# Optimization experiments

Hardware: AMD Instinct MI355X
Metric: run time of the kernel (lower is better)

## Reference

```python
import jax, jax.numpy as jnp
import numpy as np

T, N, E, F0, F1 = 8, 100000, 3200000, 16, 16


def setup_inputs() -> dict:
    key = jax.random.key(0)
    ks = jax.random.split(key, 18)
    inp = {}
    inp["X"] = jax.random.normal(ks[0], (T, N, F0), jnp.float32)
    inp["edge_row"] = jax.random.randint(ks[1], (T, E), 0, N, jnp.int32)
    inp["edge_col"] = jax.random.randint(ks[2], (T, E), 0, N, jnp.int32)
    inp["edge_val"] = jax.random.uniform(ks[3], (T, E), jnp.float32)
    inp["p"] = jax.random.normal(ks[4], (F0,), jnp.float32)
    names = ["W_Z", "U_Z", "B_Z", "W_R", "U_R", "B_R", "W_H", "U_H", "B_H", "W_init"]
    for i, n in enumerate(names):
        inp[n] = jax.random.normal(ks[5 + i], (F0, F1 if n.startswith("B") or n == "W_init" else F0), jnp.float32)
    inp["lin_w"] = jax.random.normal(ks[15], (F1,), jnp.float32)
    inp["lin_b"] = jax.random.normal(ks[16], (1,), jnp.float32)
    return inp


def reference(X, edge_row, edge_col, edge_val, p, W_Z, U_Z, B_Z, W_R, U_R, B_R, W_H, U_H, B_H, W_init, lin_w, lin_b):
    def step(W, xs):
        X_t, row, col, val = xs  # X_t: [N, F0]; row/col/val: [E]
        # summarize: topk-weighted row selection, k = F1
        y = (X_t @ p) / jnp.linalg.norm(p)              # [N]
        yk, idx = jax.lax.top_k(y, F1)                  # sorted desc, matches torch.topk
        Xs = (X_t[idx] * yk[:, None]).T                 # [F0, F1]
        # GRU on the weight matrix W: [F0, F1]
        Zg = jax.nn.sigmoid(W_Z @ Xs + U_Z @ W + B_Z)
        Rg = jax.nn.sigmoid(W_R @ Xs + U_R @ W + B_R)
        Ht = jnp.tanh(W_H @ Xs + U_H @ (Rg * W) + B_H)
        W_new = (1.0 - Zg) * W + Zg * Ht
        # sparse GCONV: (A @ X_t) @ W_new via gather + segment_sum
        AH = jax.ops.segment_sum(val[:, None] * X_t[col], row, num_segments=N)  # [N, F0]
        H_new = AH @ W_new                              # [N, F1]
        return W_new, H_new

    _, Y = jax.lax.scan(step, W_init, (X, edge_row, edge_col, edge_val))  # Y: [T, N, F1]
    return Y @ lin_w + lin_b[0]                          # [T, N]
```

## Files before the change

### kernel.cpp

```cpp
#include <hip/hip_runtime.h>
#include <stdint.h>

#define T_STEPS 8
#define N_NODES 100000
#define E_EDGES 3200000
#define NB1 250
#define CHUNK 400
#define NB3 391
#define NCAND_T 4000
#define NSLICE 8
#define ESLICE (E_EDGES / NSLICE)
#define RNG_BITS 15
#define RNG (1 << RNG_BITS)
#define NRNG 4
#define SC_BLKS (T_STEPS * NRNG * NSLICE)

__device__ __forceinline__ uint16_t f2bf(float x) {
    uint32_t b = __float_as_uint(x);
    b += 0x7FFFu + ((b >> 16) & 1u);
    return (uint16_t)(b >> 16);
}
__device__ __forceinline__ float bf2f(uint16_t u) {
    return __uint_as_float(((uint32_t)u) << 16);
}

__device__ __forceinline__ unsigned long long make_key(float v, int idx) {
    uint32_t u = __float_as_uint(v);
    u = (u & 0x80000000u) ? ~u : (u | 0x80000000u);
    return (((unsigned long long)u) << 32) | (unsigned long long)(~(uint32_t)idx);
}
__device__ __forceinline__ float key_val(unsigned long long k) {
    uint32_t u = (uint32_t)(k >> 32);
    u = (u & 0x80000000u) ? (u & 0x7FFFFFFFu) : ~u;
    return __uint_as_float(u);
}
__device__ __forceinline__ int key_idx(unsigned long long k) {
    return (int)(~(uint32_t)(k & 0xFFFFFFFFu));
}

__device__ __forceinline__ unsigned long long shfl_xor_u64(unsigned long long x, int mask) {
    uint32_t lo = (uint32_t)x, hi = (uint32_t)(x >> 32);
    lo = __shfl_xor((unsigned int)lo, mask);
    hi = __shfl_xor((unsigned int)hi, mask);
    return (((unsigned long long)hi) << 32) | lo;
}

__device__ __forceinline__ void wave_argmax(unsigned long long& m, int& mp) {
    #pragma unroll
    for (int off = 32; off; off >>= 1) {
        unsigned long long o = shfl_xor_u64(m, off);
        int op = __shfl_xor(mp, off);
        if (o > m) { m = o; mp = op; }
    }
}

__device__ __forceinline__ float dot16(const float4* __restrict__ xr, const float* w) {
    float4 a = xr[0], b = xr[1], c = xr[2], d = xr[3];
    return a.x*w[0] + a.y*w[1] + a.z*w[2] + a.w*w[3]
         + b.x*w[4] + b.y*w[5] + b.z*w[6] + b.w*w[7]
         + c.x*w[8] + c.y*w[9] + c.z*w[10] + c.w*w[11]
         + d.x*w[12] + d.y*w[13] + d.z*w[14] + d.w*w[15];
}

__global__ __launch_bounds__(256) void k_y_topk_all(const float* __restrict__ X,
                                                    const float* __restrict__ p,
                                                    unsigned long long* __restrict__ cand) {
    __shared__ unsigned long long keys[CHUNK];
    __shared__ unsigned long long wm[4];
    __shared__ int wp[4];
    int tid = threadIdx.x;
    int t = blockIdx.x / NB1;
    int b = blockIdx.x % NB1;
    const float* Xt = X + (size_t)t * N_NODES * 16;
    float pv[16];
    #pragma unroll
    for (int i = 0; i < 16; i++) pv[i] = p[i];
    float pn = 0.f;
    #pragma unroll
    for (int i = 0; i < 16; i++) pn += pv[i] * pv[i];
    float inv = 1.0f / sqrtf(pn);
    int base = b * CHUNK;
    for (int i = tid; i < CHUNK; i += 256) {
        int n = base + i;
        float y = dot16((const float4*)(Xt + (size_t)n * 16), pv) * inv;
        keys[i] = make_key(y, n);
    }
    __syncthreads();
    for (int k = 0; k < 16; k++) {
        unsigned long long m = 0ULL; int mp = -1;
        for (int i = tid; i < CHUNK; i += 256) {
            unsigned long long v = keys[i];
            if (v > m) { m = v; mp = i; }
        }
        wave_argmax(m, mp);
        if ((tid & 63) == 0) { wm[tid >> 6] = m; wp[tid >> 6] = mp; }
        __syncthreads();
        if (tid == 0) {
            unsigned long long best = wm[0]; int bp = wp[0];
            #pragma unroll
            for (int w2 = 1; w2 < 4; w2++) if (wm[w2] > best) { best = wm[w2]; bp = wp[w2]; }
            cand[(size_t)t * NCAND_T + b * 16 + k] = best;
            keys[bp] = 0ULL;
        }
        __syncthreads();
    }
}

__global__ __launch_bounds__(512) void k_merge_gru(
    const unsigned long long* __restrict__ cand,
    const float* __restrict__ X,
    const float* __restrict__ Winit,
    const float* __restrict__ W_Z, const float* __restrict__ U_Z, const float* __restrict__ B_Z,
    const float* __restrict__ W_R, const float* __restrict__ U_R, const float* __restrict__ B_R,
    const float* __restrict__ W_H, const float* __restrict__ U_H, const float* __restrict__ B_H,
    const float* __restrict__ lin_w,
    float* __restrict__ weff_g) {
    __shared__ float mWZ[256], mUZ[256], mBZ[256], mWR[256], mUR[256], mBR[256];
    __shared__ float mWH[256], mUH[256], mBH[256], mLW[16];
    __shared__ int   sidx[8][16];
    __shared__ float sval[8][16];
    __shared__ float Xs_all[8][16][16];
    __shared__ float Wcur[16][16];
    __shared__ float RgW[16][16];
    int tid = threadIdx.x;
    if (tid < 256) {
        mWZ[tid] = W_Z[tid]; mUZ[tid] = U_Z[tid]; mBZ[tid] = B_Z[tid];
        mWR[tid] = W_R[tid]; mUR[tid] = U_R[tid]; mBR[tid] = B_R[tid];
        mWH[tid] = W_H[tid]; mUH[tid] = U_H[tid]; mBH[tid] = B_H[tid];
        Wcur[tid >> 4][tid & 15] = Winit[tid];
        if (tid < 16) mLW[tid] = lin_w[tid];
    }
    {
        int w = tid >> 6, lane = tid & 63;
        const unsigned long long* ct = cand + (size_t)w * NCAND_T;
        int cb = lane * 4;
        unsigned long long h0 = 0, h1 = 0, h2 = 0, h3 = 0;
        int p0 = 0, p1 = 0, p2 = 0, p3 = 0;
        if (cb + 0 < NB1) h0 = ct[(cb + 0) * 16];
        if (cb + 1 < NB1) h1 = ct[(cb + 1) * 16];
        if (cb + 2 < NB1) h2 = ct[(cb + 2) * 16];
        if (cb + 3 < NB1) h3 = ct[(cb + 3) * 16];
        for (int k = 0; k < 16; k++) {
            unsigned long long m = h0; int pay = (lane << 2) | 0;
            if (h1 > m) { m = h1; pay = (lane << 2) | 1; }
            if (h2 > m) { m = h2; pay = (lane << 2) | 2; }
            if (h3 > m) { m = h3; pay = (lane << 2) | 3; }
            wave_argmax(m, pay);
            if (lane == 0) { sidx[w][k] = key_idx(m); sval[w][k] = key_val(m); }
            if ((pay >> 2) == lane) {
                switch (pay & 3) {
                case 0: p0++; h0 = (p0 < 16) ? ct[(cb + 0) * 16 + p0] : 0ULL; break;
                case 1: p1++; h1 = (p1 < 16) ? ct[(cb + 1) * 16 + p1] : 0ULL; break;
                case 2: p2++; h2 = (p2 < 16) ? ct[(cb + 2) * 16 + p2] : 0ULL; break;
                default: p3++; h3 = (p3 < 16) ? ct[(cb + 3) * 16 + p3] : 0ULL; break;
                }
            }
        }
    }
    __syncthreads();
    for (int e = tid; e < 8 * 256; e += 512) {
        int tt = e >> 8, kk = (e >> 4) & 15, ff = e & 15;
        Xs_all[tt][ff][kk] = X[(size_t)tt * N_NODES * 16 + (size_t)sidx[tt][kk] * 16 + ff]
                           * sval[tt][kk];
    }
    __syncthreads();
    int i = (tid & 255) >> 4, j = tid & 15;
    for (int t = 0; t < T_STEPS; t++) {
        float Zg = 0.f, wn = 0.f;
        if (tid < 256) {
            float az = 0.f, ar = 0.f, uz = 0.f, ur = 0.f;
            #pragma unroll
            for (int m = 0; m < 16; m++) {
                az += mWZ[i * 16 + m] * Xs_all[t][m][j];
                ar += mWR[i * 16 + m] * Xs_all[t][m][j];
                uz += mUZ[i * 16 + m] * Wcur[m][j];
                ur += mUR[i * 16 + m] * Wcur[m][j];
            }
            Zg = 1.0f / (1.0f + expf(-(az + uz + mBZ[i * 16 + j])));
            float Rg = 1.0f / (1.0f + expf(-(ar + ur + mBR[i * 16 + j])));
            RgW[i][j] = Rg * Wcur[i][j];
        }
        __syncthreads();
        if (tid < 256) {
            float ah = 0.f, uh = 0.f;
            #pragma unroll
            for (int m = 0; m < 16; m++) {
                ah += mWH[i * 16 + m] * Xs_all[t][m][j];
                uh += mUH[i * 16 + m] * RgW[m][j];
            }
            float Ht = tanhf(ah + uh + mBH[i * 16 + j]);
            wn = (1.0f - Zg) * Wcur[i][j] + Zg * Ht;
        }
        __syncthreads();
        if (tid < 256) Wcur[i][j] = wn;
        __syncthreads();
        if (tid < 16) {
            float acc = 0.f;
            #pragma unroll
            for (int jj = 0; jj < 16; jj++) acc += Wcur[tid][jj] * mLW[jj];
            weff_g[t * 16 + tid] = acc;
        }
        __syncthreads();
    }
}

__global__ __launch_bounds__(256) void k_s_all(const float* __restrict__ X,
                                               const float* __restrict__ weff,
                                               float* __restrict__ s) {
    int t = blockIdx.x / NB3;
    int b = blockIdx.x % NB3;
    __shared__ float w[16];
    if (threadIdx.x < 16) w[threadIdx.x] = weff[t * 16 + threadIdx.x];
    __syncthreads();
    int n = b * 256 + threadIdx.x;
    if (n < N_NODES) {
        float v = dot16((const float4*)(X + ((size_t)t * N_NODES + n) * 16), w);
        s[(size_t)t * N_NODES + n] = v;
    }
}

#define PKT(Rr, Cc, Vv) do {                                                   \
    int l0 = Rr.x - base, l1 = Rr.y - base, l2 = Rr.z - base, l3 = Rr.w - base;\
    bool b0 = (unsigned)l0 < (unsigned)RNG, b1 = (unsigned)l1 < (unsigned)RNG, \
         b2 = (unsigned)l2 < (unsigned)RNG, b3 = (unsigned)l3 < (unsigned)RNG; \
    float g0 = b0 ? st[Cc.x] : 0.f, g1 = b1 ? st[Cc.y] : 0.f,                  \
          g2 = b2 ? st[Cc.z] : 0.f, g3 = b3 ? st[Cc.w] : 0.f;                  \
    if (b0) atomicAdd(&acc[l0], Vv.x * g0);                                    \
    if (b1) atomicAdd(&acc[l1], Vv.y * g1);                                    \
    if (b2) atomicAdd(&acc[l2], Vv.z * g2);                                    \
    if (b3) atomicAdd(&acc[l3], Vv.w * g3);                                    \
} while (0)

extern "C" __global__ __launch_bounds__(1024) void k_scatter_lds(
    const int* __restrict__ erow, const int* __restrict__ ecol,
    const float* __restrict__ evalv, const float* __restrict__ s,
    uint16_t* __restrict__ rep) {
    extern __shared__ float acc[];
    const int bid = blockIdx.x;
    const int t = bid & 7;
    const int m = bid >> 3;
    const int slice = m >> 2;
    const int r = m & 3;
    const int base = r << RNG_BITS;
    const int tid = threadIdx.x;
    float4* a4 = (float4*)acc;
    #pragma unroll
    for (int q = 0; q < RNG / 4 / 1024; q++)
        a4[tid + q * 1024] = make_float4(0.f, 0.f, 0.f, 0.f);
    __syncthreads();
    const float* __restrict__ st = s + (size_t)t * N_NODES;
    const size_t eb = (size_t)t * E_EDGES + (size_t)slice * ESLICE;
    const int4* __restrict__ r4 = (const int4*)(erow + eb);
    const int4* __restrict__ c4 = (const int4*)(ecol + eb);
    const float4* __restrict__ v4 = (const float4*)(evalv + eb);
    const int n4 = ESLICE / 4;

    int i = tid;
    for (; i + 3 * 1024 < n4; i += 4 * 1024) {
        int4 R0 = r4[i], R1 = r4[i + 1024], R2 = r4[i + 2048], R3 = r4[i + 3072];
        int4 C0 = c4[i], C1 = c4[i + 1024], C2 = c4[i + 2048], C3 = c4[i + 3072];
        float4 V0 = v4[i], V1 = v4[i + 1024], V2 = v4[i + 2048], V3 = v4[i + 3072];
        PKT(R0, C0, V0);
        PKT(R1, C1, V1);
        PKT(R2, C2, V2);
        PKT(R3, C3, V3);
    }
    for (; i < n4; i += 1024) {
        int4 R0 = r4[i]; int4 C0 = c4[i]; float4 V0 = v4[i];
        PKT(R0, C0, V0);
    }
    __syncthreads();
    ushort4* rp4 = (ushort4*)(rep + (size_t)bid * RNG);
    #pragma unroll
    for (int q = 0; q < RNG / 4 / 1024; q++) {
        float4 a = a4[tid + q * 1024];
        ushort4 u;
        u.x = f2bf(a.x); u.y = f2bf(a.y); u.z = f2bf(a.z); u.w = f2bf(a.w);
        rp4[tid + q * 1024] = u;
    }
}

__global__ __launch_bounds__(256) void k_reduce(const uint16_t* __restrict__ rep,
                                                const float* __restrict__ lin_b,
                                                float* __restrict__ out) {
    int t = blockIdx.x / NB3;
    int b = blockIdx.x % NB3;
    int n = b * 256 + threadIdx.x;
    if (n >= N_NODES) return;
    int r = n >> RNG_BITS;
    int local = n & (RNG - 1);
    float acc = lin_b[0];
    #pragma unroll
    for (int sl = 0; sl < NSLICE; sl++) {
        int bid = t + 8 * (sl * NRNG + r);
        acc += bf2f(rep[(size_t)bid * RNG + local]);
    }
    out[(size_t)t * N_NODES + n] = acc;
}

extern "C" void kernel_launch(void* const* d_in, const int* in_sizes, int n_in,
                              void* d_out, int out_size, void* d_ws, size_t ws_size,
                              hipStream_t stream) {
    const float* X     = (const float*)d_in[0];
    const int*   erow  = (const int*)d_in[1];
    const int*   ecol  = (const int*)d_in[2];
    const float* evalv = (const float*)d_in[3];
    const float* p     = (const float*)d_in[4];
    const float* W_Z   = (const float*)d_in[5];
    const float* U_Z   = (const float*)d_in[6];
    const float* B_Z   = (const float*)d_in[7];
    const float* W_R   = (const float*)d_in[8];
    const float* U_R   = (const float*)d_in[9];
    const float* B_R   = (const float*)d_in[10];
    const float* W_H   = (const float*)d_in[11];
    const float* U_H   = (const float*)d_in[12];
    const float* B_H   = (const float*)d_in[13];
    const float* Winit = (const float*)d_in[14];
    const float* lin_w = (const float*)d_in[15];
    const float* lin_b = (const float*)d_in[16];
    float* out = (float*)d_out;

    size_t dynLDS = (size_t)RNG * sizeof(float);
    (void)hipFuncSetAttribute((const void*)k_scatter_lds,
                              hipFuncAttributeMaxDynamicSharedMemorySize,
                              (int)dynLDS);

    char* ws = (char*)d_ws;
    float* s    = (float*)ws;
    float* weff = (float*)(ws + 3200000);
    unsigned long long* cand = (unsigned long long*)(ws + 3201024);
    uint16_t* rep = (uint16_t*)(ws + 3457024);

    k_y_topk_all<<<T_STEPS * NB1, 256, 0, stream>>>(X, p, cand);
    k_merge_gru<<<1, 512, 0, stream>>>(cand, X, Winit,
                                       W_Z, U_Z, B_Z, W_R, U_R, B_R, W_H, U_H, B_H,
                                       lin_w, weff);
    k_s_all<<<T_STEPS * NB3, 256, 0, stream>>>(X, weff, s);
    k_scatter_lds<<<SC_BLKS, 1024, dynLDS, stream>>>(erow, ecol, evalv, s, rep);
    k_reduce<<<T_STEPS * NB3, 256, 0, stream>>>(rep, lin_b, out);
}
```

Baseline: 265.1 us.

## Split edge gather into separate pass feeding LDS scatter via contribution buffer

Adds a separate gather kernel that computes val*s[col] for every edge once and writes the products to a workspace buffer. The LDS-atomic scatter then reads only row indices and these products, instead of re-gathering s[col] in each of the 4 range blocks per slice. The fused path stays as a fallback when the workspace is too small, and the replica buffer layout is reindexed by timestep. The cost is an extra 102 MB write and re-read of the contribution buffer plus one more kernel launch.

Result: slower. 387.3 us (+46.1%).

```diff
diff --git a/kernel.cpp b/kernel.cpp
--- a/kernel.cpp
+++ b/kernel.cpp
@@ -4,6 +4,7 @@
 #define T_STEPS 8
 #define N_NODES 100000
 #define E_EDGES 3200000
+#define INT4_PER_T (E_EDGES / 4)
 #define NB1 250
 #define CHUNK 400
 #define NB3 391
@@ -219,6 +220,80 @@
     }
 }
 
+__global__ __launch_bounds__(256) void k_gather_full(const int* __restrict__ ecol,
+                                                     const float* __restrict__ evalv,
+                                                     const float* __restrict__ s,
+                                                     float* __restrict__ cbuf) {
+    int g = blockIdx.x * 256 + threadIdx.x;
+    int t = g / INT4_PER_T;
+    int i = g - t * INT4_PER_T;
+    const int4*   c4 = (const int4*)(ecol + (size_t)t * E_EDGES);
+    const float4* v4 = (const float4*)(evalv + (size_t)t * E_EDGES);
+    const float* __restrict__ st = s + (size_t)t * N_NODES;
+    int4 cc = c4[i];
+    float4 vv = v4[i];
+    float4 r;
+    r.x = vv.x * st[cc.x];
+    r.y = vv.y * st[cc.y];
+    r.z = vv.z * st[cc.z];
+    r.w = vv.w * st[cc.w];
+    ((float4*)(cbuf + (size_t)t * E_EDGES))[i] = r;
+}
+
+#define PKT2(Rr, Cc) do {                                                      \
+    int l0 = Rr.x - base, l1 = Rr.y - base, l2 = Rr.z - base, l3 = Rr.w - base;\
+    if ((unsigned)l0 < (unsigned)RNG) atomicAdd(&acc[l0], Cc.x);               \
+    if ((unsigned)l1 < (unsigned)RNG) atomicAdd(&acc[l1], Cc.y);               \
+    if ((unsigned)l2 < (unsigned)RNG) atomicAdd(&acc[l2], Cc.z);               \
+    if ((unsigned)l3 < (unsigned)RNG) atomicAdd(&acc[l3], Cc.w);               \
+} while (0)
+
+extern "C" __global__ __launch_bounds__(1024) void k_scatter_full(
+    const int* __restrict__ erow, const float* __restrict__ cbuf,
+    uint16_t* __restrict__ rep) {
+    extern __shared__ float acc[];
+    const int bid = blockIdx.x;
+    const int t = bid & 7;
+    const int m = bid >> 3;
+    const int slice = m >> 2;
+    const int r = m & 3;
+    const int base = r << RNG_BITS;
+    const int tid = threadIdx.x;
+    float4* a4 = (float4*)acc;
+    #pragma unroll
+    for (int q = 0; q < RNG / 4 / 1024; q++)
+        a4[tid + q * 1024] = make_float4(0.f, 0.f, 0.f, 0.f);
+    __syncthreads();
+    const size_t eb = (size_t)t * E_EDGES + (size_t)slice * ESLICE;
+    const int4* __restrict__ r4 = (const int4*)(erow + eb);
+    const float4* __restrict__ c4 = (const float4*)(cbuf + eb);
+    const int n4 = ESLICE / 4;
+
+    int i = tid;
+    for (; i + 3 * 1024 < n4; i += 4 * 1024) {
+        int4 R0 = r4[i], R1 = r4[i + 1024], R2 = r4[i + 2048], R3 = r4[i + 3072];
+        float4 C0 = c4[i], C1 = c4[i + 1024], C2 = c4[i + 2048], C3 = c4[i + 3072];
+        PKT2(R0, C0);
+        PKT2(R1, C1);
+        PKT2(R2, C2);
+        PKT2(R3, C3);
+    }
+    for (; i < n4; i += 1024) {
+        int4 R0 = r4[i]; float4 C0 = c4[i];
+        PKT2(R0, C0);
+    }
+    __syncthreads();
+    const int seg = t * 32 + m;
+    ushort4* rp4 = (ushort4*)(rep + (size_t)seg * RNG);
+    #pragma unroll
+    for (int q = 0; q < RNG / 4 / 1024; q++) {
+        float4 a = a4[tid + q * 1024];
+        ushort4 u;
+        u.x = f2bf(a.x); u.y = f2bf(a.y); u.z = f2bf(a.z); u.w = f2bf(a.w);
+        rp4[tid + q * 1024] = u;
+    }
+}
+
 #define PKT(Rr, Cc, Vv) do {                                                   \
     int l0 = Rr.x - base, l1 = Rr.y - base, l2 = Rr.z - base, l3 = Rr.w - base;\
     bool b0 = (unsigned)l0 < (unsigned)RNG, b1 = (unsigned)l1 < (unsigned)RNG, \
@@ -231,7 +306,7 @@
     if (b3) atomicAdd(&acc[l3], Vv.w * g3);                                    \
 } while (0)
 
-extern "C" __global__ __launch_bounds__(1024) void k_scatter_lds(
+extern "C" __global__ __launch_bounds__(1024) void k_scatter_fused(
     const int* __restrict__ erow, const int* __restrict__ ecol,
     const float* __restrict__ evalv, const float* __restrict__ s,
     uint16_t* __restrict__ rep) {
@@ -270,7 +345,8 @@
         PKT(R0, C0, V0);
     }
     __syncthreads();
-    ushort4* rp4 = (ushort4*)(rep + (size_t)bid * RNG);
+    const int seg = t * 32 + m;
+    ushort4* rp4 = (ushort4*)(rep + (size_t)seg * RNG);
     #pragma unroll
     for (int q = 0; q < RNG / 4 / 1024; q++) {
         float4 a = a4[tid + q * 1024];
@@ -280,9 +356,9 @@
     }
 }
 
-__global__ __launch_bounds__(256) void k_reduce(const uint16_t* __restrict__ rep,
-                                                const float* __restrict__ lin_b,
-                                                float* __restrict__ out) {
+__global__ __launch_bounds__(256) void k_reduce_full(const uint16_t* __restrict__ rep,
+                                                     const float* __restrict__ lin_b,
+                                                     float* __restrict__ out) {
     int t = blockIdx.x / NB3;
     int b = blockIdx.x % NB3;
     int n = b * 256 + threadIdx.x;
@@ -292,8 +368,8 @@
     float acc = lin_b[0];
     #pragma unroll
     for (int sl = 0; sl < NSLICE; sl++) {
-        int bid = t + 8 * (sl * NRNG + r);
-        acc += bf2f(rep[(size_t)bid * RNG + local]);
+        int seg = t * 32 + sl * 4 + r;
+        acc += bf2f(rep[(size_t)seg * RNG + local]);
     }
     out[(size_t)t * N_NODES + n] = acc;
 }
@@ -321,21 +397,37 @@
     float* out = (float*)d_out;
 
     size_t dynLDS = (size_t)RNG * sizeof(float);
-    (void)hipFuncSetAttribute((const void*)k_scatter_lds,
+    (void)hipFuncSetAttribute((const void*)k_scatter_full,
                               hipFuncAttributeMaxDynamicSharedMemorySize,
                               (int)dynLDS);
+    (void)hipFuncSetAttribute((const void*)k_scatter_fused,
+                              hipFuncAttributeMaxDynamicSharedMemorySize,
+                              (int)dynLDS);
 
     char* ws = (char*)d_ws;
-    float* s    = (float*)ws;
-    float* weff = (float*)(ws + 3200000);
-    unsigned long long* cand = (unsigned long long*)(ws + 3201024);
-    uint16_t* rep = (uint16_t*)(ws + 3457024);
+    const size_t S_OFF    = 0;
+    const size_t WEFF_OFF = 3200000;
+    const size_t CAND_OFF = 3200512;
+    const size_t REP_OFF  = 3456512;
+    const size_t C_OFF    = 20233728;
+    const size_t NEED_FULL = C_OFF + (size_t)T_STEPS * E_EDGES * 4;
+    float* s    = (float*)(ws + S_OFF);
+    float* weff = (float*)(ws + WEFF_OFF);
+    unsigned long long* cand = (unsigned long long*)(ws + CAND_OFF);
+    uint16_t* rep = (uint16_t*)(ws + REP_OFF);
+    float* cbuf = (float*)(ws + C_OFF);
+    const bool tierFull = (ws_size >= NEED_FULL);
 
     k_y_topk_all<<<T_STEPS * NB1, 256, 0, stream>>>(X, p, cand);
     k_merge_gru<<<1, 512, 0, stream>>>(cand, X, Winit,
                                        W_Z, U_Z, B_Z, W_R, U_R, B_R, W_H, U_H, B_H,
                                        lin_w, weff);
     k_s_all<<<T_STEPS * NB3, 256, 0, stream>>>(X, weff, s);
-    k_scatter_lds<<<SC_BLKS, 1024, dynLDS, stream>>>(erow, ecol, evalv, s, rep);
-    k_reduce<<<T_STEPS * NB3, 256, 0, stream>>>(rep, lin_b, out);
-}
+    if (tierFull) {
+        k_gather_full<<<(T_STEPS * INT4_PER_T) / 256, 256, 0, stream>>>(ecol, evalv, s, cbuf);
+        k_scatter_full<<<SC_BLKS, 1024, dynLDS, stream>>>(erow, cbuf, rep);
+    } else {
+        k_scatter_fused<<<SC_BLKS, 1024, dynLDS, stream>>>(erow, ecol, evalv, s, rep);
+    }
+    k_reduce_full<<<T_STEPS * NB3, 256, 0, stream>>>(rep, lin_b, out);
+}
```
